# Kernel optimization log

Hardware: AMD Instinct MI355X
Metric: run time of the kernel (lower is better)

## Reference

```python
import jax, jax.numpy as jnp
import numpy as np

P = 256         # ids_per_batch
K = 16          # imgs_per_id
D = 2048        # feature_dim
MARGIN = 10.0
EPS = 1e-12


def setup_inputs() -> dict:
    key = jax.random.key(0)
    features = jax.random.normal(key, (P * K, D), dtype=jnp.float32)
    # ordered batch: label i repeated K times, matching targets[0::imgs_per_id] slicing
    targets = jnp.repeat(jnp.arange(P, dtype=jnp.int64), K)
    return {"features": features, "targets": targets}


def reference(features, targets):
    # ordered path: batch == P*K, labels grouped -> reshape replaces the per-class python loop
    f = features.reshape(P, K, D)               # [P, K, D]
    centers = f.mean(axis=1)                    # [P, D] per-class mean

    # intra: euclidean dist from each center to its own K features, max per class
    intra_d2 = jnp.sum((f - centers[:, None, :]) ** 2, axis=-1)     # [P, K]
    intra_max = jnp.max(jnp.sqrt(jnp.clip(intra_d2, EPS, None)), axis=1)  # [P]

    # inter: pairwise center distances, min over other centers
    cc = jnp.sum(centers ** 2, axis=1)                              # [P]
    cd2 = cc[:, None] + cc[None, :] - 2.0 * (centers @ centers.T)   # [P, P]
    cd = jnp.sqrt(jnp.clip(cd2, EPS, None))
    cd = jnp.where(jnp.eye(P, dtype=bool), jnp.inf, cd)             # exclude self
    inter_min = jnp.min(cd, axis=1)                                 # [P]

    cluster_loss = jnp.mean(jax.nn.relu(intra_max - inter_min + MARGIN))
    return cluster_loss, intra_max, inter_min
```

## Files before the change

### kernel.cpp

```cpp
#include <hip/hip_runtime.h>
#include <math.h>

#define NP 256
#define NK 16
#define ND 2048
#define MARGIN 10.0f
#define EPSV 1e-12f

typedef short bf16x8 __attribute__((ext_vector_type(8)));
typedef float f32x4 __attribute__((ext_vector_type(4)));

static __device__ __forceinline__ unsigned short f2bf(float f) {
  unsigned u = __float_as_uint(f);
  unsigned r = (u + 0x7fffu + ((u >> 16) & 1u)) >> 16;
  return (unsigned short)r;
}

__global__ __launch_bounds__(512) void k_center_intra(
    const float* __restrict__ F, unsigned short* __restrict__ Cb,
    float* __restrict__ cc, float* __restrict__ out) {
  const int p = blockIdx.x;
  const int t = threadIdx.x;
  const int d = t * 4;

  float4 x[NK];
#pragma unroll
  for (int k = 0; k < NK; ++k)
    x[k] = *reinterpret_cast<const float4*>(&F[((size_t)(p * NK + k)) * ND + d]);

  float4 c;
  c.x = c.y = c.z = c.w = 0.f;
#pragma unroll
  for (int k = 0; k < NK; ++k) {
    c.x += x[k].x; c.y += x[k].y; c.z += x[k].z; c.w += x[k].w;
  }
  const float inv = 1.0f / 16.0f;
  c.x *= inv; c.y *= inv; c.z *= inv; c.w *= inv;

  ushort4 cb;
  cb.x = f2bf(c.x); cb.y = f2bf(c.y); cb.z = f2bf(c.z); cb.w = f2bf(c.w);
  *reinterpret_cast<ushort4*>(&Cb[(size_t)p * ND + d]) = cb;

  float ccp = c.x * c.x + c.y * c.y + c.z * c.z + c.w * c.w;

  float acc[NK];
#pragma unroll
  for (int k = 0; k < NK; ++k) {
    float dx = x[k].x - c.x, dy = x[k].y - c.y;
    float dz = x[k].z - c.z, dw = x[k].w - c.w;
    acc[k] = dx * dx + dy * dy + dz * dz + dw * dw;
  }

#pragma unroll
  for (int k = 0; k < NK; ++k) {
    float v = acc[k];
#pragma unroll
    for (int m = 32; m > 0; m >>= 1) v += __shfl_xor(v, m);
    acc[k] = v;
  }
  {
    float v = ccp;
#pragma unroll
    for (int m = 32; m > 0; m >>= 1) v += __shfl_xor(v, m);
    ccp = v;
  }

  __shared__ float red[8][NK + 1];
  const int wave = t >> 6, lane = t & 63;
  if (lane == 0) {
#pragma unroll
    for (int k = 0; k < NK; ++k) red[wave][k] = acc[k];
    red[wave][NK] = ccp;
  }
  __syncthreads();
  if (t == 0) {
    float m = 0.f;
#pragma unroll
    for (int k = 0; k < NK; ++k) {
      float s = 0.f;
#pragma unroll
      for (int w = 0; w < 8; ++w) s += red[w][k];
      m = fmaxf(m, sqrtf(fmaxf(s, EPSV)));
    }
    out[1 + p] = m;
    float s = 0.f;
#pragma unroll
    for (int w = 0; w < 8; ++w) s += red[w][NK];
    cc[p] = s;
    out[1 + NP + p] = INFINITY;
  }
}

__global__ __launch_bounds__(256) void k_gemm_inter(
    const unsigned short* __restrict__ Cb, const float* __restrict__ cc,
    float* __restrict__ out) {
  const int t = threadIdx.x;
  const int wave = t >> 6, lane = t & 63;
  const int p0 = blockIdx.x * 16;
  const int q0 = blockIdx.y * 64 + wave * 16;
  const int lr = lane & 15;
  const int kg = (lane >> 4) * 8;

  const unsigned short* ap = &Cb[(size_t)(p0 + lr) * ND + kg];
  const unsigned short* bp = &Cb[(size_t)(q0 + lr) * ND + kg];

  f32x4 acc = {0.f, 0.f, 0.f, 0.f};
#pragma unroll 8
  for (int k0 = 0; k0 < ND; k0 += 32) {
    bf16x8 a = *reinterpret_cast<const bf16x8*>(ap + k0);
    bf16x8 b = *reinterpret_cast<const bf16x8*>(bp + k0);
    acc = __builtin_amdgcn_mfma_f32_16x16x32_bf16(a, b, acc, 0, 0, 0);
  }

  const int rbase = (lane >> 4) * 4;
  const int qg = q0 + lr;
  const float ccq = cc[qg];
  float cdm[4];
#pragma unroll
  for (int r = 0; r < 4; ++r) {
    const int pg = p0 + rbase + r;
    const float cd2 = cc[pg] + ccq - 2.0f * acc[r];
    cdm[r] = (pg == qg) ? INFINITY : sqrtf(fmaxf(cd2, EPSV));
  }
#pragma unroll
  for (int r = 0; r < 4; ++r) {
#pragma unroll
    for (int m = 8; m > 0; m >>= 1) cdm[r] = fminf(cdm[r], __shfl_xor(cdm[r], m));
  }
  if (lr == 0) {
#pragma unroll
    for (int r = 0; r < 4; ++r) {
      const int pg = p0 + rbase + r;
      atomicMin(reinterpret_cast<int*>(out) + 1 + NP + pg,
                __float_as_int(cdm[r]));
    }
  }
}

__global__ __launch_bounds__(256) void k_loss(float* __restrict__ out) {
  const int t = threadIdx.x;
  const float im = out[1 + t];
  const float in_ = out[1 + NP + t];
  float v = fmaxf(im - in_ + MARGIN, 0.f);
#pragma unroll
  for (int m = 32; m > 0; m >>= 1) v += __shfl_xor(v, m);
  __shared__ float red[4];
  if ((t & 63) == 0) red[t >> 6] = v;
  __syncthreads();
  if (t == 0) out[0] = (red[0] + red[1] + red[2] + red[3]) / (float)NP;
}

extern "C" void kernel_launch(void* const* d_in, const int* in_sizes, int n_in,
                              void* d_out, int out_size, void* d_ws,
                              size_t ws_size, hipStream_t stream) {
  const float* F = (const float*)d_in[0];
  float* out = (float*)d_out;

  unsigned short* Cb = (unsigned short*)d_ws;
  float* cc = (float*)(Cb + (size_t)NP * ND);

  k_center_intra<<<NP, 512, 0, stream>>>(F, Cb, cc, out);
  k_gemm_inter<<<dim3(16, 4), 256, 0, stream>>>(Cb, cc, out);
  k_loss<<<1, 256, 0, stream>>>(out);
}
```

Baseline: 35.07 us.

## Fuse center, GEMM and loss kernels into one cooperative kernel with grid syncs

```diff
diff --git a/kernel.cpp b/kernel.cpp
--- a/kernel.cpp
+++ b/kernel.cpp
@@ -1,5 +1,8 @@
 #include <hip/hip_runtime.h>
+#include <hip/hip_cooperative_groups.h>
 #include <math.h>
+
+namespace cg = cooperative_groups;
 
 #define NP 256
 #define NK 16
@@ -12,142 +15,140 @@
 
 static __device__ __forceinline__ unsigned short f2bf(float f) {
   unsigned u = __float_as_uint(f);
-  unsigned r = (u + 0x7fffu + ((u >> 16) & 1u)) >> 16;
-  return (unsigned short)r;
+  return (unsigned short)((u + 0x7fffu + ((u >> 16) & 1u)) >> 16);
 }
 
-__global__ __launch_bounds__(512) void k_center_intra(
+__global__ __launch_bounds__(512, 2) void k_fused(
     const float* __restrict__ F, unsigned short* __restrict__ Cb,
     float* __restrict__ cc, float* __restrict__ out) {
-  const int p = blockIdx.x;
+  const int b = blockIdx.x;
   const int t = threadIdx.x;
-  const int d = t * 4;
+  const int wave = t >> 6, lane = t & 63;
 
-  float4 x[NK];
+  __shared__ float red[8][NK + 1];
+  __shared__ float red2[8][256];
+  __shared__ float red3[8];
+
+  {
+    const int p = b;
+    const int d = t * 4;
+    float4 x[NK];
 #pragma unroll
-  for (int k = 0; k < NK; ++k)
-    x[k] = *reinterpret_cast<const float4*>(&F[((size_t)(p * NK + k)) * ND + d]);
+    for (int k = 0; k < NK; ++k)
+      x[k] = *reinterpret_cast<const float4*>(
+          &F[((size_t)(p * NK + k)) * ND + d]);
+    float4 c;
+    c.x = c.y = c.z = c.w = 0.f;
+#pragma unroll
+    for (int k = 0; k < NK; ++k) {
+      c.x += x[k].x; c.y += x[k].y; c.z += x[k].z; c.w += x[k].w;
+    }
+    const float inv = 1.0f / 16.0f;
+    c.x *= inv; c.y *= inv; c.z *= inv; c.w *= inv;
 
-  float4 c;
-  c.x = c.y = c.z = c.w = 0.f;
+    ushort4 cb;
+    cb.x = f2bf(c.x); cb.y = f2bf(c.y); cb.z = f2bf(c.z); cb.w = f2bf(c.w);
+    *reinterpret_cast<ushort4*>(&Cb[(size_t)p * ND + d]) = cb;
+
+    float ccp = c.x * c.x + c.y * c.y + c.z * c.z + c.w * c.w;
+
+    float acc[NK];
 #pragma unroll
-  for (int k = 0; k < NK; ++k) {
-    c.x += x[k].x; c.y += x[k].y; c.z += x[k].z; c.w += x[k].w;
-  }
-  const float inv = 1.0f / 16.0f;
-  c.x *= inv; c.y *= inv; c.z *= inv; c.w *= inv;
-
-  ushort4 cb;
-  cb.x = f2bf(c.x); cb.y = f2bf(c.y); cb.z = f2bf(c.z); cb.w = f2bf(c.w);
-  *reinterpret_cast<ushort4*>(&Cb[(size_t)p * ND + d]) = cb;
-
-  float ccp = c.x * c.x + c.y * c.y + c.z * c.z + c.w * c.w;
-
-  float acc[NK];
+    for (int k = 0; k < NK; ++k) {
+      float dx = x[k].x - c.x, dy = x[k].y - c.y;
+      float dz = x[k].z - c.z, dw = x[k].w - c.w;
+      acc[k] = dx * dx + dy * dy + dz * dz + dw * dw;
+    }
 #pragma unroll
-  for (int k = 0; k < NK; ++k) {
-    float dx = x[k].x - c.x, dy = x[k].y - c.y;
-    float dz = x[k].z - c.z, dw = x[k].w - c.w;
-    acc[k] = dx * dx + dy * dy + dz * dz + dw * dw;
+    for (int k = 0; k < NK; ++k) {
+      float v = acc[k];
+#pragma unroll
+      for (int m = 32; m > 0; m >>= 1) v += __shfl_xor(v, m);
+      acc[k] = v;
+    }
+    {
+      float v = ccp;
+#pragma unroll
+      for (int m = 32; m > 0; m >>= 1) v += __shfl_xor(v, m);
+      ccp = v;
+    }
+    if (lane == 0) {
+#pragma unroll
+      for (int k = 0; k < NK; ++k) red[wave][k] = acc[k];
+      red[wave][NK] = ccp;
+    }
+    __syncthreads();
+    if (t == 0) {
+      float m = 0.f;
+#pragma unroll
+      for (int k = 0; k < NK; ++k) {
+        float s = 0.f;
+#pragma unroll
+        for (int w = 0; w < 8; ++w) s += red[w][k];
+        m = fmaxf(m, sqrtf(fmaxf(s, EPSV)));
+      }
+      out[1 + p] = m;
+      float s = 0.f;
+#pragma unroll
+      for (int w = 0; w < 8; ++w) s += red[w][NK];
+      cc[p] = s;
+      reinterpret_cast<int*>(out)[1 + NP + p] = 0x7f800000;
+    }
   }
 
+  cg::this_grid().sync();
+
+  {
+    const int pi = b >> 4, qi = b & 15;
+    const int lr = lane & 15;
+    const int kg = (lane >> 4) * 8;
+    const unsigned short* ap =
+        &Cb[(size_t)(pi * 16 + lr) * ND + wave * 256 + kg];
+    const unsigned short* bp =
+        &Cb[(size_t)(qi * 16 + lr) * ND + wave * 256 + kg];
+    f32x4 acc = {0.f, 0.f, 0.f, 0.f};
 #pragma unroll
-  for (int k = 0; k < NK; ++k) {
-    float v = acc[k];
+    for (int i = 0; i < 8; ++i) {
+      bf16x8 a = *reinterpret_cast<const bf16x8*>(ap + i * 32);
+      bf16x8 bb = *reinterpret_cast<const bf16x8*>(bp + i * 32);
+      acc = __builtin_amdgcn_mfma_f32_16x16x32_bf16(a, bb, acc, 0, 0, 0);
+    }
+#pragma unroll
+    for (int r = 0; r < 4; ++r) red2[wave][lane * 4 + r] = acc[r];
+    __syncthreads();
+    if (t < 256) {
+      float g = 0.f;
+#pragma unroll
+      for (int w = 0; w < 8; ++w) g += red2[w][t];
+      const int row = ((t >> 6) & 3) * 4 + (t & 3);
+      const int col = (t >> 2) & 15;
+      const int p = pi * 16 + row, q = qi * 16 + col;
+      const float cd2 = cc[p] + cc[q] - 2.0f * g;
+      float cd = (p == q) ? INFINITY : sqrtf(fmaxf(cd2, EPSV));
+#pragma unroll
+      for (int m = 4; m <= 32; m <<= 1) cd = fminf(cd, __shfl_xor(cd, m));
+      if (col == 0)
+        atomicMin(reinterpret_cast<int*>(out) + 1 + NP + p,
+                  __float_as_int(cd));
+    }
+  }
+
+  cg::this_grid().sync();
+
+  if (b == 0) {
+    float v = 0.f;
+    if (t < NP) v = fmaxf(out[1 + t] - out[1 + NP + t] + MARGIN, 0.f);
 #pragma unroll
     for (int m = 32; m > 0; m >>= 1) v += __shfl_xor(v, m);
-    acc[k] = v;
-  }
-  {
-    float v = ccp;
-#pragma unroll
-    for (int m = 32; m > 0; m >>= 1) v += __shfl_xor(v, m);
-    ccp = v;
-  }
-
-  __shared__ float red[8][NK + 1];
-  const int wave = t >> 6, lane = t & 63;
-  if (lane == 0) {
-#pragma unroll
-    for (int k = 0; k < NK; ++k) red[wave][k] = acc[k];
-    red[wave][NK] = ccp;
-  }
-  __syncthreads();
-  if (t == 0) {
-    float m = 0.f;
-#pragma unroll
-    for (int k = 0; k < NK; ++k) {
+    if (lane == 0) red3[wave] = v;
+    __syncthreads();
+    if (t == 0) {
       float s = 0.f;
 #pragma unroll
-      for (int w = 0; w < 8; ++w) s += red[w][k];
-      m = fmaxf(m, sqrtf(fmaxf(s, EPSV)));
-    }
-    out[1 + p] = m;
-    float s = 0.f;
-#pragma unroll
-    for (int w = 0; w < 8; ++w) s += red[w][NK];
-    cc[p] = s;
-    out[1 + NP + p] = INFINITY;
-  }
-}
-
-__global__ __launch_bounds__(256) void k_gemm_inter(
-    const unsigned short* __restrict__ Cb, const float* __restrict__ cc,
-    float* __restrict__ out) {
-  const int t = threadIdx.x;
-  const int wave = t >> 6, lane = t & 63;
-  const int p0 = blockIdx.x * 16;
-  const int q0 = blockIdx.y * 64 + wave * 16;
-  const int lr = lane & 15;
-  const int kg = (lane >> 4) * 8;
-
-  const unsigned short* ap = &Cb[(size_t)(p0 + lr) * ND + kg];
-  const unsigned short* bp = &Cb[(size_t)(q0 + lr) * ND + kg];
-
-  f32x4 acc = {0.f, 0.f, 0.f, 0.f};
-#pragma unroll 8
-  for (int k0 = 0; k0 < ND; k0 += 32) {
-    bf16x8 a = *reinterpret_cast<const bf16x8*>(ap + k0);
-    bf16x8 b = *reinterpret_cast<const bf16x8*>(bp + k0);
-    acc = __builtin_amdgcn_mfma_f32_16x16x32_bf16(a, b, acc, 0, 0, 0);
-  }
-
-  const int rbase = (lane >> 4) * 4;
-  const int qg = q0 + lr;
-  const float ccq = cc[qg];
-  float cdm[4];
-#pragma unroll
-  for (int r = 0; r < 4; ++r) {
-    const int pg = p0 + rbase + r;
-    const float cd2 = cc[pg] + ccq - 2.0f * acc[r];
-    cdm[r] = (pg == qg) ? INFINITY : sqrtf(fmaxf(cd2, EPSV));
-  }
-#pragma unroll
-  for (int r = 0; r < 4; ++r) {
-#pragma unroll
-    for (int m = 8; m > 0; m >>= 1) cdm[r] = fminf(cdm[r], __shfl_xor(cdm[r], m));
-  }
-  if (lr == 0) {
-#pragma unroll
-    for (int r = 0; r < 4; ++r) {
-      const int pg = p0 + rbase + r;
-      atomicMin(reinterpret_cast<int*>(out) + 1 + NP + pg,
-                __float_as_int(cdm[r]));
+      for (int w = 0; w < 8; ++w) s += red3[w];
+      out[0] = s / (float)NP;
     }
   }
-}
-
-__global__ __launch_bounds__(256) void k_loss(float* __restrict__ out) {
-  const int t = threadIdx.x;
-  const float im = out[1 + t];
-  const float in_ = out[1 + NP + t];
-  float v = fmaxf(im - in_ + MARGIN, 0.f);
-#pragma unroll
-  for (int m = 32; m > 0; m >>= 1) v += __shfl_xor(v, m);
-  __shared__ float red[4];
-  if ((t & 63) == 0) red[t >> 6] = v;
-  __syncthreads();
-  if (t == 0) out[0] = (red[0] + red[1] + red[2] + red[3]) / (float)NP;
 }
 
 extern "C" void kernel_launch(void* const* d_in, const int* in_sizes, int n_in,
@@ -159,7 +160,7 @@
   unsigned short* Cb = (unsigned short*)d_ws;
   float* cc = (float*)(Cb + (size_t)NP * ND);
 
-  k_center_intra<<<NP, 512, 0, stream>>>(F, Cb, cc, out);
-  k_gemm_inter<<<dim3(16, 4), 256, 0, stream>>>(Cb, cc, out);
-  k_loss<<<1, 256, 0, stream>>>(out);
+  void* args[4] = {(void*)&F, (void*)&Cb, (void*)&cc, (void*)&out};
+  hipLaunchCooperativeKernel((const void*)k_fused, dim3(NP), dim3(512), args,
+                             0, stream);
 }
```

Result: slower. 74.15 us (+111.4%).

## Fuse loss reduction into pairwise GEMM via last-block ticket, split MFMA accumulators

Applied to the files above, without the earlier changes.

```diff
diff --git a/kernel.cpp b/kernel.cpp
--- a/kernel.cpp
+++ b/kernel.cpp
@@ -6,27 +6,32 @@
 #define ND 2048
 #define MARGIN 10.0f
 #define EPSV 1e-12f
+#define NBLK_B 64
 
 typedef short bf16x8 __attribute__((ext_vector_type(8)));
 typedef float f32x4 __attribute__((ext_vector_type(4)));
 
 static __device__ __forceinline__ unsigned short f2bf(float f) {
   unsigned u = __float_as_uint(f);
-  unsigned r = (u + 0x7fffu + ((u >> 16) & 1u)) >> 16;
-  return (unsigned short)r;
+  return (unsigned short)((u + 0x7fffu + ((u >> 16) & 1u)) >> 16);
 }
 
 __global__ __launch_bounds__(512) void k_center_intra(
     const float* __restrict__ F, unsigned short* __restrict__ Cb,
-    float* __restrict__ cc, float* __restrict__ out) {
+    float* __restrict__ cc, int* __restrict__ ticket,
+    float* __restrict__ out) {
   const int p = blockIdx.x;
   const int t = threadIdx.x;
+  const int wave = t >> 6, lane = t & 63;
   const int d = t * 4;
 
   float4 x[NK];
 #pragma unroll
   for (int k = 0; k < NK; ++k)
     x[k] = *reinterpret_cast<const float4*>(&F[((size_t)(p * NK + k)) * ND + d]);
+#pragma unroll
+  for (int k = 0; k < NK; ++k)
+    asm volatile("" : "+v"(x[k].x), "+v"(x[k].y), "+v"(x[k].z), "+v"(x[k].w));
 
   float4 c;
   c.x = c.y = c.z = c.w = 0.f;
@@ -66,7 +71,6 @@
   }
 
   __shared__ float red[8][NK + 1];
-  const int wave = t >> 6, lane = t & 63;
   if (lane == 0) {
 #pragma unroll
     for (int k = 0; k < NK; ++k) red[wave][k] = acc[k];
@@ -87,38 +91,49 @@
 #pragma unroll
     for (int w = 0; w < 8; ++w) s += red[w][NK];
     cc[p] = s;
-    out[1 + NP + p] = INFINITY;
+    reinterpret_cast<int*>(out)[1 + NP + p] = 0x7f800000;
+    if (p == 0) atomicExch(ticket, 0);
   }
 }
 
-__global__ __launch_bounds__(256) void k_gemm_inter(
+__global__ __launch_bounds__(256) void k_pair_loss(
     const unsigned short* __restrict__ Cb, const float* __restrict__ cc,
-    float* __restrict__ out) {
+    int* __restrict__ ticket, float* __restrict__ out) {
   const int t = threadIdx.x;
   const int wave = t >> 6, lane = t & 63;
-  const int p0 = blockIdx.x * 16;
-  const int q0 = blockIdx.y * 64 + wave * 16;
+  const int tile = blockIdx.x * 4 + wave;
+  const int pi = tile >> 4, qi = tile & 15;
   const int lr = lane & 15;
   const int kg = (lane >> 4) * 8;
 
-  const unsigned short* ap = &Cb[(size_t)(p0 + lr) * ND + kg];
-  const unsigned short* bp = &Cb[(size_t)(q0 + lr) * ND + kg];
+  const unsigned short* ap = &Cb[(size_t)(pi * 16 + lr) * ND + kg];
+  const unsigned short* bp = &Cb[(size_t)(qi * 16 + lr) * ND + kg];
 
-  f32x4 acc = {0.f, 0.f, 0.f, 0.f};
-#pragma unroll 8
-  for (int k0 = 0; k0 < ND; k0 += 32) {
-    bf16x8 a = *reinterpret_cast<const bf16x8*>(ap + k0);
-    bf16x8 b = *reinterpret_cast<const bf16x8*>(bp + k0);
-    acc = __builtin_amdgcn_mfma_f32_16x16x32_bf16(a, b, acc, 0, 0, 0);
+  f32x4 a0 = {0.f, 0.f, 0.f, 0.f}, a1 = a0, a2 = a0, a3 = a0;
+#pragma unroll
+  for (int i = 0; i < 16; ++i) {
+    bf16x8 av0 = *reinterpret_cast<const bf16x8*>(ap + i * 128);
+    bf16x8 bv0 = *reinterpret_cast<const bf16x8*>(bp + i * 128);
+    bf16x8 av1 = *reinterpret_cast<const bf16x8*>(ap + i * 128 + 32);
+    bf16x8 bv1 = *reinterpret_cast<const bf16x8*>(bp + i * 128 + 32);
+    bf16x8 av2 = *reinterpret_cast<const bf16x8*>(ap + i * 128 + 64);
+    bf16x8 bv2 = *reinterpret_cast<const bf16x8*>(bp + i * 128 + 64);
+    bf16x8 av3 = *reinterpret_cast<const bf16x8*>(ap + i * 128 + 96);
+    bf16x8 bv3 = *reinterpret_cast<const bf16x8*>(bp + i * 128 + 96);
+    a0 = __builtin_amdgcn_mfma_f32_16x16x32_bf16(av0, bv0, a0, 0, 0, 0);
+    a1 = __builtin_amdgcn_mfma_f32_16x16x32_bf16(av1, bv1, a1, 0, 0, 0);
+    a2 = __builtin_amdgcn_mfma_f32_16x16x32_bf16(av2, bv2, a2, 0, 0, 0);
+    a3 = __builtin_amdgcn_mfma_f32_16x16x32_bf16(av3, bv3, a3, 0, 0, 0);
   }
+  f32x4 acc = a0 + a1 + a2 + a3;
 
   const int rbase = (lane >> 4) * 4;
-  const int qg = q0 + lr;
+  const int qg = qi * 16 + lr;
   const float ccq = cc[qg];
   float cdm[4];
 #pragma unroll
   for (int r = 0; r < 4; ++r) {
-    const int pg = p0 + rbase + r;
+    const int pg = pi * 16 + rbase + r;
     const float cd2 = cc[pg] + ccq - 2.0f * acc[r];
     cdm[r] = (pg == qg) ? INFINITY : sqrtf(fmaxf(cd2, EPSV));
   }
@@ -129,25 +144,28 @@
   }
   if (lr == 0) {
 #pragma unroll
-    for (int r = 0; r < 4; ++r) {
-      const int pg = p0 + rbase + r;
-      atomicMin(reinterpret_cast<int*>(out) + 1 + NP + pg,
+    for (int r = 0; r < 4; ++r)
+      atomicMin(reinterpret_cast<int*>(out) + 1 + NP + pi * 16 + rbase + r,
                 __float_as_int(cdm[r]));
-    }
   }
-}
 
-__global__ __launch_bounds__(256) void k_loss(float* __restrict__ out) {
-  const int t = threadIdx.x;
-  const float im = out[1 + t];
-  const float in_ = out[1 + NP + t];
-  float v = fmaxf(im - in_ + MARGIN, 0.f);
+  __syncthreads();
+  __threadfence();
+  __shared__ int my_ticket;
+  if (t == 0) my_ticket = atomicAdd(ticket, 1);
+  __syncthreads();
+  if (my_ticket == NBLK_B - 1) {
+    const float im = out[1 + t];
+    const int bits = atomicOr(reinterpret_cast<int*>(out) + 1 + NP + t, 0);
+    const float in_ = __int_as_float(bits);
+    float v = fmaxf(im - in_ + MARGIN, 0.f);
 #pragma unroll
-  for (int m = 32; m > 0; m >>= 1) v += __shfl_xor(v, m);
-  __shared__ float red[4];
-  if ((t & 63) == 0) red[t >> 6] = v;
-  __syncthreads();
-  if (t == 0) out[0] = (red[0] + red[1] + red[2] + red[3]) / (float)NP;
+    for (int m = 32; m > 0; m >>= 1) v += __shfl_xor(v, m);
+    __shared__ float red[4];
+    if (lane == 0) red[wave] = v;
+    __syncthreads();
+    if (t == 0) out[0] = (red[0] + red[1] + red[2] + red[3]) / (float)NP;
+  }
 }
 
 extern "C" void kernel_launch(void* const* d_in, const int* in_sizes, int n_in,
@@ -158,8 +176,8 @@
 
   unsigned short* Cb = (unsigned short*)d_ws;
   float* cc = (float*)(Cb + (size_t)NP * ND);
+  int* ticket = (int*)(cc + NP);
 
-  k_center_intra<<<NP, 512, 0, stream>>>(F, Cb, cc, out);
-  k_gemm_inter<<<dim3(16, 4), 256, 0, stream>>>(Cb, cc, out);
-  k_loss<<<1, 256, 0, stream>>>(out);
+  k_center_intra<<<NP, 512, 0, stream>>>(F, Cb, cc, ticket, out);
+  k_pair_loss<<<NBLK_B, 256, 0, stream>>>(Cb, cc, ticket, out);
 }
```

New measurement: 34.41 us. About the same (-1.9%).
